# Kernel optimization log

Measured on AMD Instinct MI355X. Metric: run time of the kernel, lower is better.

Reference implementation:

```python
import jax, jax.numpy as jnp
import numpy as np

N, T, S, H, NCLS = 256, 300, 150, 100, 60

def _lstm_params(key, in_dim, hid, scale=0.05):
    k1, k2, k3, k4 = jax.random.split(key, 4)
    return (jax.random.normal(k1, (4 * hid, in_dim), jnp.float32) * scale,
            jax.random.normal(k2, (4 * hid, hid), jnp.float32) * scale,
            jax.random.normal(k3, (4 * hid,), jnp.float32) * scale,
            jax.random.normal(k4, (4 * hid,), jnp.float32) * scale)

def setup_inputs() -> dict:
    key = jax.random.key(0)
    ks = jax.random.split(key, 12)
    inp = {"x": jax.random.normal(ks[0], (N, T, S), jnp.float32)}
    for pref, k in (("rot", ks[1]), ("tr", ks[2])):
        Wih, Whh, bih, bhh = _lstm_params(k, S, H)
        inp[pref + "_Wih"], inp[pref + "_Whh"] = Wih, Whh
        inp[pref + "_bih"], inp[pref + "_bhh"] = bih, bhh
    # rotation/translation fc: zero-initialized in the original weights_init,
    # but we use small random values so the rotation path is exercised.
    inp["rot_fcW"] = jax.random.normal(ks[3], (3, H), jnp.float32) * 0.05
    inp["rot_fcb"] = jax.random.normal(ks[4], (3,), jnp.float32) * 0.05
    inp["tr_fcW"] = jax.random.normal(ks[5], (3, H), jnp.float32) * 0.05
    inp["tr_fcb"] = jax.random.normal(ks[6], (3,), jnp.float32) * 0.05
    for l in range(3):  # main 3-layer LSTM: layer0 in=150, layers1/2 in=100
        Wih, Whh, bih, bhh = _lstm_params(ks[7 + l], S if l == 0 else H, H)
        inp[f"main_Wih{l}"], inp[f"main_Whh{l}"] = Wih, Whh
        inp[f"main_bih{l}"], inp[f"main_bhh{l}"] = bih, bhh
    inp["main_fcW"] = jax.random.normal(ks[10], (NCLS, H), jnp.float32) * 0.05
    inp["main_fcb"] = jax.random.normal(ks[11], (NCLS,), jnp.float32) * 0.05
    return inp

def lstm(x, Wih, Whh, bih, bhh):
    # x: (N, T, in) -> (N, T, H); PyTorch gate order i,f,g,o
    n, t, _ = x.shape
    hid = Whh.shape[1]
    xg = jnp.einsum('nti,gi->ntg', x, Wih) + bih + bhh  # (N,T,4H)
    def step(carry, g):
        h, c = carry
        g = g + h @ Whh.T
        i, f, gg, o = jnp.split(g, 4, axis=-1)
        c = jax.nn.sigmoid(f) * c + jax.nn.sigmoid(i) * jnp.tanh(gg)
        h = jax.nn.sigmoid(o) * jnp.tanh(c)
        return (h, c), h
    init = (jnp.zeros((n, hid), x.dtype), jnp.zeros((n, hid), x.dtype))
    _, hs = jax.lax.scan(step, init, xg.transpose(1, 0, 2))
    return hs.transpose(1, 0, 2)

def rotation_matrices(ang):
    # ang: (N,T,3). Faithful to the original (including sin(-a) placements).
    a, b, c = ang[..., 0], ang[..., 1], ang[..., 2]
    ca, sa = jnp.cos(a), jnp.sin(a)
    cb, sb = jnp.cos(b), jnp.sin(b)
    cc, sc = jnp.cos(c), jnp.sin(c)
    z = jnp.zeros_like(a); o = jnp.ones_like(a)
    Rx = jnp.stack([o, z, z, z, ca, sa, z, -sa, ca], -1).reshape(*a.shape, 3, 3)
    Ry = jnp.stack([cb, z, -sb, z, o, z, sb, z, cb], -1).reshape(*a.shape, 3, 3)
    Rz = jnp.stack([cc, sc, z, -sc, cc, z, z, z, o], -1).reshape(*a.shape, 3, 3)
    return jnp.einsum('ntij,ntjk,ntkl->ntil', Rz, Ry, Rx)

def varnn_forward(x,
                  rot_Wih, rot_Whh, rot_bih, rot_bhh, rot_fcW, rot_fcb,
                  tr_Wih, tr_Whh, tr_bih, tr_bhh, tr_fcW, tr_fcb,
                  main_Wih0, main_Whh0, main_bih0, main_bhh0,
                  main_Wih1, main_Whh1, main_bih1, main_bhh1,
                  main_Wih2, main_Whh2, main_bih2, main_bhh2,
                  main_fcW, main_fcb):
    n, t, _ = x.shape
    # eval mode: dropout layers are identity
    rot = lstm(x, rot_Wih, rot_Whh, rot_bih, rot_bhh) @ rot_fcW.T + rot_fcb   # (N,T,3)
    tr = lstm(x, tr_Wih, tr_Whh, tr_bih, tr_bhh) @ tr_fcW.T + tr_fcb          # (N,T,3)
    # .item() in the original detaches the rotation angles from the graph
    R = rotation_matrices(jax.lax.stop_gradient(rot))                          # (N,T,3,3)
    pts = x.reshape(n, t, 50, 3) - tr[:, :, None, :]                           # (N,T,50,3)
    xr = jnp.einsum('ntij,ntpj->ntpi', R, pts).reshape(n, t, 150)
    h = lstm(xr, main_Wih0, main_Whh0, main_bih0, main_bhh0)
    h = lstm(h, main_Wih1, main_Whh1, main_bih1, main_bhh1)
    h = lstm(h, main_Wih2, main_Whh2, main_bih2, main_bhh2)
    logits = h @ main_fcW.T + main_fcb                                         # (N,T,60)
    return jax.nn.softmax(logits.mean(axis=1), axis=1)                         # (N,60)

def reference(x,
              rot_Wih, rot_Whh, rot_bih, rot_bhh, rot_fcW, rot_fcb,
              tr_Wih, tr_Whh, tr_bih, tr_bhh, tr_fcW, tr_fcb,
              main_Wih0, main_Whh0, main_bih0, main_bhh0,
              main_Wih1, main_Whh1, main_bih1, main_bhh1,
              main_Wih2, main_Whh2, main_bih2, main_bhh2,
              main_fcW, main_fcb):
    return varnn_forward(x,
                         rot_Wih, rot_Whh, rot_bih, rot_bhh, rot_fcW, rot_fcb,
                         tr_Wih, tr_Whh, tr_bih, tr_bhh, tr_fcW, tr_fcb,
                         main_Wih0, main_Whh0, main_bih0, main_bhh0,
                         main_Wih1, main_Whh1, main_bih1, main_bhh1,
                         main_Wih2, main_Whh2, main_bih2, main_bhh2,
                         main_fcW, main_fcb)
```

## Files before the change

### kernel.cpp

```cpp
#include <hip/hip_runtime.h>
#include <cstddef>

#define NB   256
#define TT   300
#define SS   150
#define HH   100
#define G4   400
#define NCLS 60

__device__ __forceinline__ float sigf(float x) {
    float e = __expf(-x);
    return 1.f / (1.f + e);
}
__device__ __forceinline__ float tanh_fast(float x) {
    float e = __expf(2.f * x);
    return 1.f - 2.f / (e + 1.f);
}

template<int K>
__global__ __launch_bounds__(256, 2) void gemm_inproj(
    const float* __restrict__ A, const float* __restrict__ W,
    const float* __restrict__ bih, const float* __restrict__ bhh,
    float* __restrict__ C)
{
    __shared__ float As[K][64];
    __shared__ float Bs[K][64];
    const int m0 = blockIdx.x * 64;
    const int n0 = blockIdx.y * 64;
    const int tid = threadIdx.x;
    const int r = tid & 63;
    constexpr int K2 = K / 2;

    for (int i = tid; i < 64 * K2; i += 256) {
        int c2 = i >> 6;
        float2 v = *(const float2*)(A + (size_t)(m0 + r) * K + 2 * c2);
        As[2 * c2][r] = v.x;
        As[2 * c2 + 1][r] = v.y;
    }
    {
        int g = n0 + r;
        if (g < G4) {
            for (int i = tid; i < 64 * K2; i += 256) {
                int c2 = i >> 6;
                float2 v = *(const float2*)(W + (size_t)g * K + 2 * c2);
                Bs[2 * c2][r] = v.x;
                Bs[2 * c2 + 1][r] = v.y;
            }
        } else {
            for (int i = tid; i < 64 * K2; i += 256) {
                int c2 = i >> 6;
                Bs[2 * c2][r] = 0.f;
                Bs[2 * c2 + 1][r] = 0.f;
            }
        }
    }
    __syncthreads();

    const int tx = tid & 15, ty = tid >> 4;
    float acc[4][4] = {};
#pragma unroll 10
    for (int k = 0; k < K; ++k) {
        float4 a = *(const float4*)&As[k][ty * 4];
        float4 b = *(const float4*)&Bs[k][tx * 4];
        acc[0][0] += a.x * b.x; acc[0][1] += a.x * b.y; acc[0][2] += a.x * b.z; acc[0][3] += a.x * b.w;
        acc[1][0] += a.y * b.x; acc[1][1] += a.y * b.y; acc[1][2] += a.y * b.z; acc[1][3] += a.y * b.w;
        acc[2][0] += a.z * b.x; acc[2][1] += a.z * b.y; acc[2][2] += a.z * b.z; acc[2][3] += a.z * b.w;
        acc[3][0] += a.w * b.x; acc[3][1] += a.w * b.y; acc[3][2] += a.w * b.z; acc[3][3] += a.w * b.w;
    }

    const int g0 = n0 + tx * 4;
    if (g0 + 3 < G4) {
        float b0 = bih[g0] + bhh[g0];
        float b1 = bih[g0 + 1] + bhh[g0 + 1];
        float b2 = bih[g0 + 2] + bhh[g0 + 2];
        float b3 = bih[g0 + 3] + bhh[g0 + 3];
#pragma unroll
        for (int i = 0; i < 4; ++i) {
            float4 o;
            o.x = acc[i][0] + b0; o.y = acc[i][1] + b1;
            o.z = acc[i][2] + b2; o.w = acc[i][3] + b3;
            *(float4*)(C + (size_t)(m0 + ty * 4 + i) * G4 + g0) = o;
        }
    }
}

template<int MODE>
__global__ __launch_bounds__(512, 1) void lstm_rec(
    const float* __restrict__ xgA, const float* __restrict__ xgB,
    const float* __restrict__ WhhA, const float* __restrict__ WhhB,
    const float* __restrict__ fwA, const float* __restrict__ fbA,
    const float* __restrict__ fwB, const float* __restrict__ fbB,
    float* __restrict__ oA, float* __restrict__ oB)
{
    constexpr int FSZ = (MODE == 2) ? (NCLS * HH + NCLS) : (3 * HH + 4);
    __shared__ float h_lds[HH];
    __shared__ float gate_lds[G4];
    __shared__ float fcw[FSZ];

    const int tid = threadIdx.x;
    int n = blockIdx.x;
    const float* xg = xgA;
    const float* whh = WhhA;
    const float* fw = fwA;
    const float* fb = fbA;
    float* op = oA;
    if (MODE == 0 && blockIdx.x >= NB) {
        n = blockIdx.x - NB;
        xg = xgB; whh = WhhB; fw = fwB; fb = fbB; op = oB;
    }

    float4 w[25];
    if (tid < G4) {
        const float4* wr = (const float4*)(whh + (size_t)tid * HH);
#pragma unroll
        for (int i = 0; i < 25; ++i) w[i] = wr[i];
    }
    if (tid < HH) h_lds[tid] = 0.f;
    if (MODE == 0) {
        for (int i = tid; i < 3 * HH; i += 512) fcw[i] = fw[i];
        if (tid < 3) fcw[3 * HH + tid] = fb[tid];
    }
    if (MODE == 2) {
        for (int i = tid; i < NCLS * HH; i += 512) fcw[i] = fw[i];
        if (tid < NCLS) fcw[NCLS * HH + tid] = fb[tid];
    }
    float c = 0.f, hsum = 0.f;
    __syncthreads();

    const float* xgn = xg + (size_t)n * TT * G4 + tid;
    float x0 = 0.f, x1 = 0.f;
    if (tid < G4) { x0 = xgn[0]; x1 = xgn[G4]; }

    for (int t = 0; t < TT; ++t) {
        float acc = x0;
        x0 = x1;
        if (tid < G4 && t + 2 < TT) x1 = xgn[(size_t)(t + 2) * G4];

        if (tid < G4) {
            const float4* h4 = (const float4*)h_lds;
            float a0 = 0.f, a1 = 0.f, a2 = 0.f, a3 = 0.f;
#pragma unroll
            for (int i = 0; i < 24; i += 4) {
                float4 p = h4[i], q = h4[i + 1], s = h4[i + 2], u = h4[i + 3];
                a0 += p.x * w[i].x + p.y * w[i].y + p.z * w[i].z + p.w * w[i].w;
                a1 += q.x * w[i + 1].x + q.y * w[i + 1].y + q.z * w[i + 1].z + q.w * w[i + 1].w;
                a2 += s.x * w[i + 2].x + s.y * w[i + 2].y + s.z * w[i + 2].z + s.w * w[i + 2].w;
                a3 += u.x * w[i + 3].x + u.y * w[i + 3].y + u.z * w[i + 3].z + u.w * w[i + 3].w;
            }
            float4 p = h4[24];
            a0 += p.x * w[24].x + p.y * w[24].y + p.z * w[24].z + p.w * w[24].w;
            acc += (a0 + a1) + (a2 + a3);
            gate_lds[tid] = acc;
        }
        __syncthreads();
        if (tid < HH) {
            float ig = sigf(gate_lds[tid]);
            float fg = sigf(gate_lds[tid + HH]);
            float gg = tanh_fast(gate_lds[tid + 2 * HH]);
            float og = sigf(gate_lds[tid + 3 * HH]);
            c = fg * c + ig * gg;
            float h = og * tanh_fast(c);
            h_lds[tid] = h;
            if (MODE == 1) op[((size_t)n * TT + t) * HH + tid] = h;
            if (MODE == 2) hsum += h;
        }
        __syncthreads();
        if (MODE == 0 && tid < 64) {
            float p0 = 0.f, p1 = 0.f, p2 = 0.f;
            for (int k = tid; k < HH; k += 64) {
                float hk = h_lds[k];
                p0 += hk * fcw[k];
                p1 += hk * fcw[HH + k];
                p2 += hk * fcw[2 * HH + k];
            }
#pragma unroll
            for (int s = 32; s; s >>= 1) {
                p0 += __shfl_xor(p0, s);
                p1 += __shfl_xor(p1, s);
                p2 += __shfl_xor(p2, s);
            }
            if (tid == 0) {
                size_t o = ((size_t)n * TT + t) * 3;
                op[o] = p0 + fcw[3 * HH];
                op[o + 1] = p1 + fcw[3 * HH + 1];
                op[o + 2] = p2 + fcw[3 * HH + 2];
            }
        }
    }

    if (MODE == 2) {
        if (tid < HH) h_lds[tid] = hsum * (1.f / TT);
        __syncthreads();
        if (tid < 64) {
            float logit = -3.0e38f;
            if (tid < NCLS) {
                float a = fcw[NCLS * HH + tid];
#pragma unroll
                for (int k = 0; k < HH; ++k) a += h_lds[k] * fcw[tid * HH + k];
                logit = a;
            }
            float mx = logit;
#pragma unroll
            for (int s = 32; s; s >>= 1) mx = fmaxf(mx, __shfl_xor(mx, s));
            float e = (tid < NCLS) ? __expf(logit - mx) : 0.f;
            float sum = e;
#pragma unroll
            for (int s = 32; s; s >>= 1) sum += __shfl_xor(sum, s);
            if (tid < NCLS) op[(size_t)n * NCLS + tid] = e / sum;
        }
    }
}

__global__ __launch_bounds__(256) void transform_pts(
    const float* __restrict__ x, const float* __restrict__ rot,
    const float* __restrict__ tr, float* __restrict__ xr)
{
    const int idx = blockIdx.x * 4 + (threadIdx.x >> 6);
    const int lane = threadIdx.x & 63;
    const float* ang = rot + (size_t)idx * 3;
    float a = ang[0], b = ang[1], cg = ang[2];
    float ca = cosf(a), sa = sinf(a);
    float cb = cosf(b), sb = sinf(b);
    float cc = cosf(cg), sc = sinf(cg);
    float R00 = cc * cb, R01 = cc * sb * sa + sc * ca, R02 = -cc * sb * ca + sc * sa;
    float R10 = -sc * cb, R11 = -sc * sb * sa + cc * ca, R12 = sc * sb * ca + cc * sa;
    float R20 = sb, R21 = -cb * sa, R22 = cb * ca;
    float t0 = tr[(size_t)idx * 3], t1 = tr[(size_t)idx * 3 + 1], t2 = tr[(size_t)idx * 3 + 2];
    if (lane < 50) {
        const float* xp = x + (size_t)idx * SS + lane * 3;
        float p0 = xp[0] - t0, p1 = xp[1] - t1, p2 = xp[2] - t2;
        float* o = xr + (size_t)idx * SS + lane * 3;
        o[0] = R00 * p0 + R01 * p1 + R02 * p2;
        o[1] = R10 * p0 + R11 * p1 + R12 * p2;
        o[2] = R20 * p0 + R21 * p1 + R22 * p2;
    }
}

extern "C" void kernel_launch(void* const* d_in, const int* in_sizes, int n_in,
                              void* d_out, int out_size, void* d_ws, size_t ws_size,
                              hipStream_t stream)
{
    const float* x       = (const float*)d_in[0];
    const float* rot_Wih = (const float*)d_in[1];
    const float* rot_Whh = (const float*)d_in[2];
    const float* rot_bih = (const float*)d_in[3];
    const float* rot_bhh = (const float*)d_in[4];
    const float* tr_Wih  = (const float*)d_in[5];
    const float* tr_Whh  = (const float*)d_in[6];
    const float* tr_bih  = (const float*)d_in[7];
    const float* tr_bhh  = (const float*)d_in[8];
    const float* rot_fcW = (const float*)d_in[9];
    const float* rot_fcb = (const float*)d_in[10];
    const float* tr_fcW  = (const float*)d_in[11];
    const float* tr_fcb  = (const float*)d_in[12];
    const float* W0 = (const float*)d_in[13];
    const float* U0 = (const float*)d_in[14];
    const float* b0i = (const float*)d_in[15];
    const float* b0h = (const float*)d_in[16];
    const float* W1 = (const float*)d_in[17];
    const float* U1 = (const float*)d_in[18];
    const float* b1i = (const float*)d_in[19];
    const float* b1h = (const float*)d_in[20];
    const float* W2 = (const float*)d_in[21];
    const float* U2 = (const float*)d_in[22];
    const float* b2i = (const float*)d_in[23];
    const float* b2h = (const float*)d_in[24];
    const float* fcW = (const float*)d_in[25];
    const float* fcb = (const float*)d_in[26];
    float* out = (float*)d_out;

    float* ws = (float*)d_ws;
    float* xgA  = ws;
    float* xgB  = ws + 30720000ull;
    float* rotA = ws + 61440000ull;
    float* trO  = ws + 61670400ull;
    float* xr = xgA;
    float* h0 = xgA + 11520000ull;
    float* h1 = xgA + 19200000ull;

    dim3 gg(1200, 7), bb(256);
    gemm_inproj<150><<<gg, bb, 0, stream>>>(x, rot_Wih, rot_bih, rot_bhh, xgA);
    gemm_inproj<150><<<gg, bb, 0, stream>>>(x, tr_Wih, tr_bih, tr_bhh, xgB);
    lstm_rec<0><<<512, 512, 0, stream>>>(xgA, xgB, rot_Whh, tr_Whh,
                                         rot_fcW, rot_fcb, tr_fcW, tr_fcb,
                                         rotA, trO);
    transform_pts<<<19200, 256, 0, stream>>>(x, rotA, trO, xr);
    gemm_inproj<150><<<gg, bb, 0, stream>>>(xr, W0, b0i, b0h, xgB);
    lstm_rec<1><<<256, 512, 0, stream>>>(xgB, nullptr, U0, nullptr,
                                         nullptr, nullptr, nullptr, nullptr,
                                         h0, nullptr);
    gemm_inproj<100><<<gg, bb, 0, stream>>>(h0, W1, b1i, b1h, xgB);
    lstm_rec<1><<<256, 512, 0, stream>>>(xgB, nullptr, U1, nullptr,
                                         nullptr, nullptr, nullptr, nullptr,
                                         h1, nullptr);
    gemm_inproj<100><<<gg, bb, 0, stream>>>(h1, W2, b2i, b2h, xgB);
    lstm_rec<2><<<256, 512, 0, stream>>>(xgB, nullptr, U2, nullptr,
                                         fcW, fcb, nullptr, nullptr,
                                         out, nullptr);
}
```

Baseline: 3.089 ms.

## Split LSTM recurrent matvec over K halves with readlane broadcast of h

The recurrent kernel now uses 14 waves (896 threads): each gate row's dot product over the hidden state is split into two K-halves handled by different waves. Partial sums go to LDS and are added in the cell update. Each wave loads a 64-element slice of h into a register and broadcasts it with readlane instead of reading float4s from LDS. This halves per-thread weight registers and the serial FMA chain per step, at the cost of more threads, an extra LDS partial buffer and scalar readlane traffic.

```diff
diff --git a/kernel.cpp b/kernel.cpp
--- a/kernel.cpp
+++ b/kernel.cpp
@@ -15,6 +15,9 @@
 __device__ __forceinline__ float tanh_fast(float x) {
     float e = __expf(2.f * x);
     return 1.f - 2.f / (e + 1.f);
+}
+__device__ __forceinline__ float rlane(float v, int l) {
+    return __int_as_float(__builtin_amdgcn_readlane(__float_as_int(v), l));
 }
 
 template<int K>
@@ -85,7 +88,7 @@
 }
 
 template<int MODE>
-__global__ __launch_bounds__(512, 1) void lstm_rec(
+__global__ __launch_bounds__(896, 1) void lstm_rec(
     const float* __restrict__ xgA, const float* __restrict__ xgB,
     const float* __restrict__ WhhA, const float* __restrict__ WhhB,
     const float* __restrict__ fwA, const float* __restrict__ fbA,
@@ -93,8 +96,8 @@
     float* __restrict__ oA, float* __restrict__ oB)
 {
     constexpr int FSZ = (MODE == 2) ? (NCLS * HH + NCLS) : (3 * HH + 4);
-    __shared__ float h_lds[HH];
-    __shared__ float gate_lds[G4];
+    __shared__ float h_lds[128];
+    __shared__ float part_lds[800];
     __shared__ float fcw[FSZ];
 
     const int tid = threadIdx.x;
@@ -109,55 +112,84 @@
         xg = xgB; whh = WhhB; fw = fwB; fb = fbB; op = oB;
     }
 
-    float4 w[25];
-    if (tid < G4) {
-        const float4* wr = (const float4*)(whh + (size_t)tid * HH);
-#pragma unroll
-        for (int i = 0; i < 25; ++i) w[i] = wr[i];
-    }
-    if (tid < HH) h_lds[tid] = 0.f;
+    const int wave = tid >> 6, lane = tid & 63;
+    const int halfk = (wave >= 7) ? 1 : 0;
+    const int g = (halfk ? wave - 7 : wave) * 64 + lane;
+    const bool act = (g < G4);
+    const int k0 = halfk ? 52 : 0;
+
+    float4 wq[13];
+    if (act) {
+        const float4* wr = (const float4*)(whh + (size_t)g * HH + k0);
+        const int cnt = halfk ? 12 : 13;
+#pragma unroll 13
+        for (int j = 0; j < 13; ++j)
+            if (j < cnt) wq[j] = wr[j];
+    }
+    if (halfk) wq[12] = make_float4(0.f, 0.f, 0.f, 0.f);
+
+    if (tid < 128) h_lds[tid] = 0.f;
     if (MODE == 0) {
-        for (int i = tid; i < 3 * HH; i += 512) fcw[i] = fw[i];
+        for (int i = tid; i < 3 * HH; i += 896) fcw[i] = fw[i];
         if (tid < 3) fcw[3 * HH + tid] = fb[tid];
     }
     if (MODE == 2) {
-        for (int i = tid; i < NCLS * HH; i += 512) fcw[i] = fw[i];
+        for (int i = tid; i < NCLS * HH; i += 896) fcw[i] = fw[i];
         if (tid < NCLS) fcw[NCLS * HH + tid] = fb[tid];
     }
     float c = 0.f, hsum = 0.f;
     __syncthreads();
 
-    const float* xgn = xg + (size_t)n * TT * G4 + tid;
+    const bool act0 = act && (halfk == 0);
+    const float* xgn = xg + (size_t)n * TT * G4 + g;
     float x0 = 0.f, x1 = 0.f;
-    if (tid < G4) { x0 = xgn[0]; x1 = xgn[G4]; }
+    if (act0) { x0 = xgn[0]; x1 = xgn[G4]; }
 
     for (int t = 0; t < TT; ++t) {
-        float acc = x0;
+        float hreg = h_lds[k0 + lane];
+
+        float a0 = act0 ? x0 : 0.f;
+        float a1 = 0.f, a2 = 0.f, a3 = 0.f;
         x0 = x1;
-        if (tid < G4 && t + 2 < TT) x1 = xgn[(size_t)(t + 2) * G4];
-
-        if (tid < G4) {
-            const float4* h4 = (const float4*)h_lds;
-            float a0 = 0.f, a1 = 0.f, a2 = 0.f, a3 = 0.f;
-#pragma unroll
-            for (int i = 0; i < 24; i += 4) {
-                float4 p = h4[i], q = h4[i + 1], s = h4[i + 2], u = h4[i + 3];
-                a0 += p.x * w[i].x + p.y * w[i].y + p.z * w[i].z + p.w * w[i].w;
-                a1 += q.x * w[i + 1].x + q.y * w[i + 1].y + q.z * w[i + 1].z + q.w * w[i + 1].w;
-                a2 += s.x * w[i + 2].x + s.y * w[i + 2].y + s.z * w[i + 2].z + s.w * w[i + 2].w;
-                a3 += u.x * w[i + 3].x + u.y * w[i + 3].y + u.z * w[i + 3].z + u.w * w[i + 3].w;
-            }
-            float4 p = h4[24];
-            a0 += p.x * w[24].x + p.y * w[24].y + p.z * w[24].z + p.w * w[24].w;
-            acc += (a0 + a1) + (a2 + a3);
-            gate_lds[tid] = acc;
-        }
+        if (act0 && t + 2 < TT) x1 = xgn[(size_t)(t + 2) * G4];
+
+#pragma unroll
+        for (int j = 0; j < 13; j += 4) {
+            float4 q0 = wq[j];
+            a0 += rlane(hreg, 4 * j + 0) * q0.x;
+            a0 += rlane(hreg, 4 * j + 1) * q0.y;
+            a0 += rlane(hreg, 4 * j + 2) * q0.z;
+            a0 += rlane(hreg, 4 * j + 3) * q0.w;
+            if (j + 1 < 13) {
+                float4 q1 = wq[j + 1];
+                a1 += rlane(hreg, 4 * j + 4) * q1.x;
+                a1 += rlane(hreg, 4 * j + 5) * q1.y;
+                a1 += rlane(hreg, 4 * j + 6) * q1.z;
+                a1 += rlane(hreg, 4 * j + 7) * q1.w;
+            }
+            if (j + 2 < 13) {
+                float4 q2 = wq[j + 2];
+                a2 += rlane(hreg, 4 * j + 8) * q2.x;
+                a2 += rlane(hreg, 4 * j + 9) * q2.y;
+                a2 += rlane(hreg, 4 * j + 10) * q2.z;
+                a2 += rlane(hreg, 4 * j + 11) * q2.w;
+            }
+            if (j + 3 < 13) {
+                float4 q3 = wq[j + 3];
+                a3 += rlane(hreg, 4 * j + 12) * q3.x;
+                a3 += rlane(hreg, 4 * j + 13) * q3.y;
+                a3 += rlane(hreg, 4 * j + 14) * q3.z;
+                a3 += rlane(hreg, 4 * j + 15) * q3.w;
+            }
+        }
+        if (act) part_lds[halfk * G4 + g] = (a0 + a1) + (a2 + a3);
         __syncthreads();
+
         if (tid < HH) {
-            float ig = sigf(gate_lds[tid]);
-            float fg = sigf(gate_lds[tid + HH]);
-            float gg = tanh_fast(gate_lds[tid + 2 * HH]);
-            float og = sigf(gate_lds[tid + 3 * HH]);
+            float ig = sigf(part_lds[tid] + part_lds[G4 + tid]);
+            float fg = sigf(part_lds[tid + HH] + part_lds[G4 + tid + HH]);
+            float gg = tanh_fast(part_lds[tid + 2 * HH] + part_lds[G4 + tid + 2 * HH]);
+            float og = sigf(part_lds[tid + 3 * HH] + part_lds[G4 + tid + 3 * HH]);
             c = fg * c + ig * gg;
             float h = og * tanh_fast(c);
             h_lds[tid] = h;
@@ -165,6 +197,7 @@
             if (MODE == 2) hsum += h;
         }
         __syncthreads();
+
         if (MODE == 0 && tid < 64) {
             float p0 = 0.f, p1 = 0.f, p2 = 0.f;
             for (int k = tid; k < HH; k += 64) {
@@ -281,20 +314,20 @@
     dim3 gg(1200, 7), bb(256);
     gemm_inproj<150><<<gg, bb, 0, stream>>>(x, rot_Wih, rot_bih, rot_bhh, xgA);
     gemm_inproj<150><<<gg, bb, 0, stream>>>(x, tr_Wih, tr_bih, tr_bhh, xgB);
-    lstm_rec<0><<<512, 512, 0, stream>>>(xgA, xgB, rot_Whh, tr_Whh,
+    lstm_rec<0><<<512, 896, 0, stream>>>(xgA, xgB, rot_Whh, tr_Whh,
                                          rot_fcW, rot_fcb, tr_fcW, tr_fcb,
                                          rotA, trO);
     transform_pts<<<19200, 256, 0, stream>>>(x, rotA, trO, xr);
     gemm_inproj<150><<<gg, bb, 0, stream>>>(xr, W0, b0i, b0h, xgB);
-    lstm_rec<1><<<256, 512, 0, stream>>>(xgB, nullptr, U0, nullptr,
+    lstm_rec<1><<<256, 896, 0, stream>>>(xgB, nullptr, U0, nullptr,
                                          nullptr, nullptr, nullptr, nullptr,
                                          h0, nullptr);
     gemm_inproj<100><<<gg, bb, 0, stream>>>(h0, W1, b1i, b1h, xgB);
-    lstm_rec<1><<<256, 512, 0, stream>>>(xgB, nullptr, U1, nullptr,
+    lstm_rec<1><<<256, 896, 0, stream>>>(xgB, nullptr, U1, nullptr,
                                          nullptr, nullptr, nullptr, nullptr,
                                          h1, nullptr);
     gemm_inproj<100><<<gg, bb, 0, stream>>>(h1, W2, b2i, b2h, xgB);
-    lstm_rec<2><<<256, 512, 0, stream>>>(xgB, nullptr, U2, nullptr,
+    lstm_rec<2><<<256, 896, 0, stream>>>(xgB, nullptr, U2, nullptr,
                                          fcW, fcb, nullptr, nullptr,
                                          out, nullptr);
 }
```

Measured after the change: 2.725 ms. 1.13x faster.

## Stage recurrent weights in LDS and broadcast hidden state via readlane

Applied to the files above, without the earlier changes.

Moves the per-thread recurrent weight rows from registers into a full LDS copy of Whh. The hidden state is now broadcast across the wave with readlane instead of vector LDS reads. The goal is to free registers, with weights re-read from LDS every timestep in exchange. The final FC weights are now read from global memory so the LDS budget fits.

```diff
diff --git a/kernel.cpp b/kernel.cpp
--- a/kernel.cpp
+++ b/kernel.cpp
@@ -15,6 +15,9 @@
 __device__ __forceinline__ float tanh_fast(float x) {
     float e = __expf(2.f * x);
     return 1.f - 2.f / (e + 1.f);
+}
+__device__ __forceinline__ float rlane(float v, int l) {
+    return __int_as_float(__builtin_amdgcn_readlane(__float_as_int(v), l));
 }
 
 template<int K>
@@ -85,15 +88,16 @@
 }
 
 template<int MODE>
-__global__ __launch_bounds__(512, 1) void lstm_rec(
+__global__ __launch_bounds__(512) void lstm_rec(
     const float* __restrict__ xgA, const float* __restrict__ xgB,
     const float* __restrict__ WhhA, const float* __restrict__ WhhB,
     const float* __restrict__ fwA, const float* __restrict__ fbA,
     const float* __restrict__ fwB, const float* __restrict__ fbB,
     float* __restrict__ oA, float* __restrict__ oB)
 {
-    constexpr int FSZ = (MODE == 2) ? (NCLS * HH + NCLS) : (3 * HH + 4);
-    __shared__ float h_lds[HH];
+    constexpr int FSZ = (MODE == 0) ? (3 * HH + 4) : 4;
+    __shared__ float wlds[G4 * HH];
+    __shared__ float h_lds[128];
     __shared__ float gate_lds[G4];
     __shared__ float fcw[FSZ];
 
@@ -109,50 +113,57 @@
         xg = xgB; whh = WhhB; fw = fwB; fb = fbB; op = oB;
     }
 
-    float4 w[25];
-    if (tid < G4) {
-        const float4* wr = (const float4*)(whh + (size_t)tid * HH);
-#pragma unroll
-        for (int i = 0; i < 25; ++i) w[i] = wr[i];
-    }
-    if (tid < HH) h_lds[tid] = 0.f;
+    {
+        const float4* src = (const float4*)whh;
+        float4* dst = (float4*)wlds;
+        for (int i = tid; i < G4 * HH / 4; i += 512) dst[i] = src[i];
+    }
+    if (tid < 128) h_lds[tid] = 0.f;
     if (MODE == 0) {
         for (int i = tid; i < 3 * HH; i += 512) fcw[i] = fw[i];
         if (tid < 3) fcw[3 * HH + tid] = fb[tid];
     }
-    if (MODE == 2) {
-        for (int i = tid; i < NCLS * HH; i += 512) fcw[i] = fw[i];
-        if (tid < NCLS) fcw[NCLS * HH + tid] = fb[tid];
-    }
     float c = 0.f, hsum = 0.f;
     __syncthreads();
 
-    const float* xgn = xg + (size_t)n * TT * G4 + tid;
+    const int lane = tid & 63;
+    const int g = tid;
+    const bool act = (g < G4);
+    const int gsafe = act ? g : 0;
+    const float4* wrow = (const float4*)(wlds + gsafe * HH);
+
+    const float* xgn = xg + (size_t)n * TT * G4 + g;
     float x0 = 0.f, x1 = 0.f;
-    if (tid < G4) { x0 = xgn[0]; x1 = xgn[G4]; }
+    if (act) { x0 = xgn[0]; x1 = xgn[G4]; }
 
     for (int t = 0; t < TT; ++t) {
-        float acc = x0;
+        float hlo = h_lds[lane];
+        float hhi = h_lds[64 + lane];
+
+        float s0 = act ? x0 : 0.f;
+        float s1 = 0.f, s2 = 0.f, s3 = 0.f;
         x0 = x1;
-        if (tid < G4 && t + 2 < TT) x1 = xgn[(size_t)(t + 2) * G4];
-
-        if (tid < G4) {
-            const float4* h4 = (const float4*)h_lds;
-            float a0 = 0.f, a1 = 0.f, a2 = 0.f, a3 = 0.f;
-#pragma unroll
-            for (int i = 0; i < 24; i += 4) {
-                float4 p = h4[i], q = h4[i + 1], s = h4[i + 2], u = h4[i + 3];
-                a0 += p.x * w[i].x + p.y * w[i].y + p.z * w[i].z + p.w * w[i].w;
-                a1 += q.x * w[i + 1].x + q.y * w[i + 1].y + q.z * w[i + 1].z + q.w * w[i + 1].w;
-                a2 += s.x * w[i + 2].x + s.y * w[i + 2].y + s.z * w[i + 2].z + s.w * w[i + 2].w;
-                a3 += u.x * w[i + 3].x + u.y * w[i + 3].y + u.z * w[i + 3].z + u.w * w[i + 3].w;
-            }
-            float4 p = h4[24];
-            a0 += p.x * w[24].x + p.y * w[24].y + p.z * w[24].z + p.w * w[24].w;
-            acc += (a0 + a1) + (a2 + a3);
-            gate_lds[tid] = acc;
-        }
+        if (act && t + 2 < TT) x1 = xgn[(size_t)(t + 2) * G4];
+
+#pragma unroll
+        for (int j = 0; j < 25; ++j) {
+            float4 wv = wrow[j];
+            const int k = 4 * j;
+            float h0 = (k + 0 < 64) ? rlane(hlo, (k + 0) & 63) : rlane(hhi, (k + 0) & 63);
+            float h1 = (k + 1 < 64) ? rlane(hlo, (k + 1) & 63) : rlane(hhi, (k + 1) & 63);
+            float h2 = (k + 2 < 64) ? rlane(hlo, (k + 2) & 63) : rlane(hhi, (k + 2) & 63);
+            float h3 = (k + 3 < 64) ? rlane(hlo, (k + 3) & 63) : rlane(hhi, (k + 3) & 63);
+            switch (j & 3) {
+            case 0: s0 = fmaf(h0, wv.x, fmaf(h1, wv.y, fmaf(h2, wv.z, fmaf(h3, wv.w, s0)))); break;
+            case 1: s1 = fmaf(h0, wv.x, fmaf(h1, wv.y, fmaf(h2, wv.z, fmaf(h3, wv.w, s1)))); break;
+            case 2: s2 = fmaf(h0, wv.x, fmaf(h1, wv.y, fmaf(h2, wv.z, fmaf(h3, wv.w, s2)))); break;
+            default: s3 = fmaf(h0, wv.x, fmaf(h1, wv.y, fmaf(h2, wv.z, fmaf(h3, wv.w, s3)))); break;
+            }
+        }
+
+        if (act) gate_lds[g] = (s0 + s1) + (s2 + s3);
         __syncthreads();
+
         if (tid < HH) {
             float ig = sigf(gate_lds[tid]);
             float fg = sigf(gate_lds[tid + HH]);
@@ -165,6 +176,7 @@
             if (MODE == 2) hsum += h;
         }
         __syncthreads();
+
         if (MODE == 0 && tid < 64) {
             float p0 = 0.f, p1 = 0.f, p2 = 0.f;
             for (int k = tid; k < HH; k += 64) {
@@ -194,9 +206,10 @@
         if (tid < 64) {
             float logit = -3.0e38f;
             if (tid < NCLS) {
-                float a = fcw[NCLS * HH + tid];
-#pragma unroll
-                for (int k = 0; k < HH; ++k) a += h_lds[k] * fcw[tid * HH + k];
+                float a = fb[tid];
+                const float* fr = fw + tid * HH;
+#pragma unroll 10
+                for (int k = 0; k < HH; ++k) a += h_lds[k] * fr[k];
                 logit = a;
             }
             float mx = logit;
```

Result: slower. 3.397 ms (+10.0%).
